# Kernel tuning notes

Hardware: AMD Instinct MI355X
Metric: run time of the kernel (lower is better)

Reference implementation:

```python
import jax, jax.numpy as jnp
import numpy as np

NUM = 512
SIGMA = 0.2

def approx_heaviside(x):
    # ApproxHeaviside forward: hard step (0/1); sigma only affects the surrogate gradient.
    return (x > 0).astype(x.dtype)

def setup_inputs() -> dict:
    key = jax.random.key(0)
    k1, k2 = jax.random.split(key)
    inputs = jax.random.normal(k1, (8, 4096, NUM), dtype=jnp.float32)
    w = jax.random.normal(k2, (NUM, NUM), dtype=jnp.float32) * 0.02
    b = jnp.zeros((NUM,), dtype=jnp.float32)
    return {"inputs": inputs, "w": w, "b": b}

def reference(inputs, w, b):
    # zero the diagonal of w (fill_diagonal_(0))
    w1 = w * (1.0 - jnp.eye(NUM, dtype=w.dtype))
    # inhib = rinputs @ w1 + b over all tokens, vectorized
    inhib = jnp.einsum('bsn,nm->bsm', inputs, w1) + b
    gate = approx_heaviside(inhib)
    # diag_embed(inhib) then matmul == elementwise multiply by the gate
    return inputs * gate
```

## Files before the change

### kernel.cpp

```cpp
#include <hip/hip_runtime.h>
#include <stdint.h>


#define NUMD 512
#define EPS 1e-3f
#define FIXCAP (1u << 20)
#define LCAP 2048u
#define SA 4096.0f
#define SW 8192.0f
#define INV_S (1.0f / 33554432.0f)
#define TILE_F16 4096
#define SLAB_F16 (16 * TILE_F16)

typedef _Float16 f16;
typedef _Float16 f16x8 __attribute__((ext_vector_type(8)));
typedef float    f32x4 __attribute__((ext_vector_type(4)));

#define GLOAD_LDS16(g, l)                                                      \
  __builtin_amdgcn_global_load_lds(                                            \
      (const __attribute__((address_space(1))) void*)(g),                      \
      (__attribute__((address_space(3))) void*)(l), 16, 0, 0)

__global__ __launch_bounds__(256) void prep(
    const float* __restrict__ W, float* __restrict__ Wt,
    f16* __restrict__ WtH, f16* __restrict__ WtL, unsigned* __restrict__ cnt,
    const float* __restrict__ A, f16* __restrict__ AH, f16* __restrict__ AL,
    int M, int nAblocks)
{
    const int b = blockIdx.x;
    if (b < NUMD) {
        const int n = b;
        if (n == 0 && threadIdx.x == 0) *cnt = 0;
        const int slab = n >> 7, rn = n & 127;
        const int srow = (rn >> 1) & 3;
        for (int k = threadIdx.x; k < NUMD; k += 256) {
            float v = W[(size_t)k * NUMD + n];
            if (k == n) v = 0.0f;
            Wt[(size_t)n * NUMD + k] = v;
            const float vs = v * SW;
            f16 h  = (f16)vs;
            f16 lo = (f16)(vs - (float)h);
            const int kt = k >> 5, kk = k & 31, c = kk >> 3, e = kk & 7;
            const int p = c ^ srow;
            const size_t off = (size_t)slab * SLAB_F16 + (size_t)kt * TILE_F16
                             + rn * 32 + p * 8 + e;
            WtH[off] = h; WtL[off] = lo;
        }
    } else {
        const long total = (long)M * 64;
        for (long i = (long)(b - NUMD) * 256 + threadIdx.x; i < total;
             i += (long)nAblocks * 256) {
            const int m = (int)(i >> 6), ch = (int)(i & 63);
            const int kt = ch >> 2, c = ch & 3;
            const int slab = m >> 7, rm = m & 127;
            const int p = c ^ ((rm >> 1) & 3);
            const float* src = A + (size_t)m * NUMD + (ch << 3);
            float4 a0 = *(const float4*)src;
            float4 a1 = *(const float4*)(src + 4);
            const float av[8] = {a0.x, a0.y, a0.z, a0.w, a1.x, a1.y, a1.z, a1.w};
            f16x8 h, lo;
#pragma unroll
            for (int e = 0; e < 8; ++e) {
                const float as = av[e] * SA;
                f16 hv = (f16)as;
                h[e]  = hv;
                lo[e] = (f16)(as - (float)hv);
            }
            const size_t off = (size_t)slab * SLAB_F16 + (size_t)kt * TILE_F16
                             + rm * 32 + p * 8;
            *(f16x8*)(AH + off) = h;
            *(f16x8*)(AL + off) = lo;
        }
    }
}

__global__ __launch_bounds__(256, 2) void li_mfma(
    const float* __restrict__ A,
    const f16* __restrict__ AH, const f16* __restrict__ AL,
    const f16* __restrict__ WtH, const f16* __restrict__ WtL,
    const float* __restrict__ bias,
    float* __restrict__ out,
    unsigned* __restrict__ cnt, unsigned* __restrict__ list,
    int M, int cpx)
{
    __shared__ __align__(16) f16 lds[2][4][128][32];
    __shared__ unsigned lcnt, lbase;

    const int tid = threadIdx.x;
    const int l   = tid & 63;
    const int wv  = tid >> 6;
    const int wr  = wv >> 1;
    const int wc  = wv & 1;
    const int lG  = l >> 4;
    const int lM  = l & 15;

    int w = blockIdx.x;
    if (cpx) { const int xcd = w & 7, c = w >> 3; w = xcd * cpx + c; }
    const int m0  = (w >> 2) * 128;
    const int n0b = (w & 3) * 128;

    const size_t aOff = ((size_t)(m0 >> 7) * SLAB_F16) * 2 + wv * 2048 + l * 16;
    const size_t bOff = ((size_t)(n0b >> 7) * SLAB_F16) * 2 + wv * 2048 + l * 16;
    const char* pAH = (const char*)AH;
    const char* pAL = (const char*)AL;
    const char* pBH = (const char*)WtH;
    const char* pBL = (const char*)WtL;

#define STAGE(nb, ktb) do {                                                    \
    GLOAD_LDS16(pAH + aOff + (ktb),        &lds[nb][0][wv * 32][0]);           \
    GLOAD_LDS16(pAH + aOff + (ktb) + 1024, &lds[nb][0][wv * 32 + 16][0]);      \
    GLOAD_LDS16(pAL + aOff + (ktb),        &lds[nb][1][wv * 32][0]);           \
    GLOAD_LDS16(pAL + aOff + (ktb) + 1024, &lds[nb][1][wv * 32 + 16][0]);      \
    GLOAD_LDS16(pBH + bOff + (ktb),        &lds[nb][2][wv * 32][0]);           \
    GLOAD_LDS16(pBH + bOff + (ktb) + 1024, &lds[nb][2][wv * 32 + 16][0]);      \
    GLOAD_LDS16(pBL + bOff + (ktb),        &lds[nb][3][wv * 32][0]);           \
    GLOAD_LDS16(pBL + bOff + (ktb) + 1024, &lds[nb][3][wv * 32 + 16][0]);      \
  } while (0)

    int aRd[4], bRd[4];
#pragma unroll
    for (int f = 0; f < 4; ++f) {
        const int mr = wr * 64 + f * 16 + lM;
        aRd[f] = mr * 64 + ((lG ^ ((mr >> 1) & 3)) << 4);
        const int nr = wc * 64 + f * 16 + lM;
        bRd[f] = nr * 64 + ((lG ^ ((nr >> 1) & 3)) << 4);
    }

    f32x4 acc[4][4];
#pragma unroll
    for (int i = 0; i < 4; ++i)
#pragma unroll
        for (int j = 0; j < 4; ++j) acc[i][j] = f32x4{0.f, 0.f, 0.f, 0.f};

    STAGE(0, 0);

    const int NT = NUMD / 32;
    for (int kt = 0; kt < NT; ++kt) {
        const int cur = kt & 1;
        __syncthreads();
        if (kt + 1 < NT) STAGE(cur ^ 1, (size_t)(kt + 1) * 8192);

        const char* PAH = (const char*)&lds[cur][0][0][0];
        const char* PAL = (const char*)&lds[cur][1][0][0];
        const char* PBH = (const char*)&lds[cur][2][0][0];
        const char* PBL = (const char*)&lds[cur][3][0][0];

        f16x8 bh[4], bl[4];
#pragma unroll
        for (int fj = 0; fj < 4; ++fj) {
            bh[fj] = *(const f16x8*)(PBH + bRd[fj]);
            bl[fj] = *(const f16x8*)(PBL + bRd[fj]);
        }
        __builtin_amdgcn_s_setprio(1);
#pragma unroll
        for (int fi = 0; fi < 4; ++fi) {
            const f16x8 ah = *(const f16x8*)(PAH + aRd[fi]);
            const f16x8 al = *(const f16x8*)(PAL + aRd[fi]);
#pragma unroll
            for (int fj = 0; fj < 4; ++fj) {
                acc[fi][fj] = __builtin_amdgcn_mfma_f32_16x16x32_f16(ah, bh[fj], acc[fi][fj], 0, 0, 0);
                acc[fi][fj] = __builtin_amdgcn_mfma_f32_16x16x32_f16(ah, bl[fj], acc[fi][fj], 0, 0, 0);
                acc[fi][fj] = __builtin_amdgcn_mfma_f32_16x16x32_f16(al, bh[fj], acc[fi][fj], 0, 0, 0);
            }
        }
        __builtin_amdgcn_s_setprio(0);
    }

    __syncthreads();
    unsigned* lbuf = (unsigned*)&lds[0][0][0][0];
    if (tid == 0) lcnt = 0;
    __syncthreads();

#pragma unroll
    for (int fj = 0; fj < 4; ++fj) {
        const int n = n0b + wc * 64 + fj * 16 + lM;
        const float bvj = bias[n];
#pragma unroll
        for (int fi = 0; fi < 4; ++fi) {
            const int mb = m0 + wr * 64 + fi * 16 + lG * 4;
#pragma unroll
            for (int r = 0; r < 4; ++r) {
                const size_t idx = (size_t)(mb + r) * NUMD + n;
                const float inh = acc[fi][fj][r] * INV_S + bvj;
                const float x = A[idx];
                out[idx] = (inh > 0.0f) ? x : 0.0f;
                if (__builtin_fabsf(inh) <= EPS) {
                    unsigned p = atomicAdd(&lcnt, 1u);
                    if (p < LCAP) lbuf[p] = (unsigned)idx;
                }
            }
        }
    }

    __syncthreads();
    if (tid == 0) {
        unsigned nf = lcnt; if (nf > LCAP) nf = LCAP;
        lbase = atomicAdd(cnt, nf);
    }
    __syncthreads();
    {
        unsigned nf = lcnt; if (nf > LCAP) nf = LCAP;
        for (unsigned i = tid; i < nf; i += 256) {
            const unsigned p = lbase + i;
            if (p < FIXCAP) list[p] = lbuf[i];
        }
    }
#undef STAGE
}

__global__ __launch_bounds__(256) void fixup(
    const float* __restrict__ A, const float* __restrict__ Wt,
    const float* __restrict__ bias, float* __restrict__ out,
    const unsigned* __restrict__ cnt, const unsigned* __restrict__ list,
    unsigned total)
{
    unsigned nfix = *cnt;
    if (nfix > FIXCAP) nfix = FIXCAP;
    for (unsigned e = blockIdx.x * blockDim.x + threadIdx.x; e < nfix;
         e += gridDim.x * blockDim.x) {
        const unsigned code = list[e];
        if (code >= total) continue;
        const int n = (int)(code & 511);
        const float* ar = A  + (size_t)(code >> 9) * NUMD;
        const float* wr = Wt + (size_t)n * NUMD;
        float s = 0.0f;
#pragma unroll 8
        for (int k = 0; k < NUMD; ++k)
            s = fmaf(ar[k], wr[k], s);
        const float inh = s + bias[n];
        out[code] = (inh > 0.0f) ? A[code] : 0.0f;
    }
}

#define BM 128
#define BN 256
#define BK 16
#define TM 8
#define TN 16
#define NTF (NUMD / BK)

__global__ __launch_bounds__(256) void zero_diag_kernel(
    const float* __restrict__ W, float* __restrict__ Wz)
{
    const int f = (int)(blockIdx.x * blockDim.x + threadIdx.x) * 4;
    const int row = f >> 9, col0 = f & 511;
    float4 v = *(const float4*)(W + f);
    if (row == col0 + 0) v.x = 0.0f;
    if (row == col0 + 1) v.y = 0.0f;
    if (row == col0 + 2) v.z = 0.0f;
    if (row == col0 + 3) v.w = 0.0f;
    *(float4*)(Wz + f) = v;
}

template<bool ZDIAG>
__global__ __launch_bounds__(256, 1) void li_gemm_fp32(
    const float* __restrict__ A, const float* __restrict__ Wm,
    const float* __restrict__ bias, float* __restrict__ out, int M)
{
    __shared__ __align__(16) float As[2][BM][BK];
    __shared__ __align__(16) float Bs[2][BK][BN];
    const int tid = threadIdx.x, lane = tid & 63, wv = tid >> 6;
    const int tc = tid & 15, tr = tid >> 4;
    const int m0 = blockIdx.x * BM, n0 = blockIdx.y * BN;
    const int am0 = wv * 32 + (lane >> 2), am1 = am0 + 16;
    const int q0 = ((lane & 3) ^ ((am0 >> 3) & 3)) << 2;
    const int q1 = ((lane & 3) ^ ((am1 >> 3) & 3)) << 2;
    const float* aSrc0 = A + (size_t)(m0 + am0) * NUMD + q0;
    const float* aSrc1 = A + (size_t)(m0 + am1) * NUMD + q1;
    const float* wSrc = Wm + (size_t)(wv * 4) * NUMD + n0 + lane * 4;
    float acc[TM][TN];
#pragma unroll
    for (int i = 0; i < TM; ++i)
#pragma unroll
        for (int j = 0; j < TN; ++j) acc[i][j] = 0.0f;
    GLOAD_LDS16(aSrc0, &As[0][wv * 32][0]);
    GLOAD_LDS16(aSrc1, &As[0][wv * 32 + 16][0]);
#pragma unroll
    for (int r = 0; r < 4; ++r)
        GLOAD_LDS16(wSrc + (size_t)r * NUMD, &Bs[0][wv * 4 + r][0]);
    aSrc0 += BK; aSrc1 += BK; wSrc += (size_t)BK * NUMD;
    for (int kt = 0; kt < NTF; ++kt) {
        const int cur = kt & 1;
        __syncthreads();
        if (kt + 1 < NTF) {
            const int nb = cur ^ 1;
            GLOAD_LDS16(aSrc0, &As[nb][wv * 32][0]);
            GLOAD_LDS16(aSrc1, &As[nb][wv * 32 + 16][0]);
#pragma unroll
            for (int r = 0; r < 4; ++r)
                GLOAD_LDS16(wSrc + (size_t)r * NUMD, &Bs[nb][wv * 4 + r][0]);
            aSrc0 += BK; aSrc1 += BK; wSrc += (size_t)BK * NUMD;
        }
        if (ZDIAG) {
            const int kk = kt * BK;
            if (tid < BK) {
                const int col = kk + tid - n0;
                if (col >= 0 && col < BN) Bs[cur][tid][col] = 0.0f;
            }
            __syncthreads();
        }
#pragma unroll
        for (int g = 0; g < 4; ++g) {
            float4 af[TM];
#pragma unroll
            for (int i = 0; i < TM; ++i) {
                const int m = tr * TM + i;
                af[i] = *(const float4*)&As[cur][m][(g ^ ((m >> 3) & 3)) << 2];
            }
#pragma unroll
            for (int dk = 0; dk < 4; ++dk) {
                float b[TN];
#pragma unroll
                for (int c = 0; c < 4; ++c) {
                    float4 b4 = *(const float4*)&Bs[cur][g * 4 + dk][tc * 4 + 64 * c];
                    b[4*c+0] = b4.x; b[4*c+1] = b4.y; b[4*c+2] = b4.z; b[4*c+3] = b4.w;
                }
#pragma unroll
                for (int i = 0; i < TM; ++i) {
                    const float a = ((const float*)&af[i])[dk];
#pragma unroll
                    for (int j = 0; j < TN; ++j) acc[i][j] = fmaf(a, b[j], acc[i][j]);
                }
            }
        }
    }
    float bv[TN];
#pragma unroll
    for (int c = 0; c < 4; ++c) {
        float4 b4 = *(const float4*)(bias + n0 + tc * 4 + 64 * c);
        bv[4*c+0] = b4.x; bv[4*c+1] = b4.y; bv[4*c+2] = b4.z; bv[4*c+3] = b4.w;
    }
#pragma unroll
    for (int i = 0; i < TM; ++i) {
        const int gm = m0 + tr * TM + i;
        const float* inrow = A + (size_t)gm * NUMD + n0 + tc * 4;
        float* orow = out + (size_t)gm * NUMD + n0 + tc * 4;
#pragma unroll
        for (int c = 0; c < 4; ++c) {
            float4 x = *(const float4*)(inrow + 64 * c);
            float4 o;
            o.x = (acc[i][4*c+0] + bv[4*c+0] > 0.0f) ? x.x : 0.0f;
            o.y = (acc[i][4*c+1] + bv[4*c+1] > 0.0f) ? x.y : 0.0f;
            o.z = (acc[i][4*c+2] + bv[4*c+2] > 0.0f) ? x.z : 0.0f;
            o.w = (acc[i][4*c+3] + bv[4*c+3] > 0.0f) ? x.w : 0.0f;
            *(float4*)(orow + 64 * c) = o;
        }
    }
}

extern "C" void kernel_launch(void* const* d_in, const int* in_sizes, int n_in,
                              void* d_out, int out_size, void* d_ws, size_t ws_size,
                              hipStream_t stream) {
    const float* A    = (const float*)d_in[0];
    const float* W    = (const float*)d_in[1];
    const float* bias = (const float*)d_in[2];
    float* out        = (float*)d_out;
    const int M = in_sizes[0] / NUMD;

    const size_t szA  = (size_t)M * NUMD * 2;
    const size_t need = (2u << 20) + 2 * szA + 1024 + 4 * (size_t)FIXCAP;

    if (ws_size >= need) {
        char* wsb = (char*)d_ws;
        float*    Wt   = (float*)wsb;
        f16*      WtH  = (f16*)(wsb + (1u << 20));
        f16*      WtL  = (f16*)(wsb + (1u << 20) + (512u << 10));
        f16*      AH   = (f16*)(wsb + (2u << 20));
        f16*      AL   = (f16*)(wsb + (2u << 20) + szA);
        unsigned* cnt  = (unsigned*)(wsb + (2u << 20) + 2 * szA);
        unsigned* list = cnt + 256;

        const int nAblocks = 4096;
        prep<<<dim3(NUMD + nAblocks), 256, 0, stream>>>(
            W, Wt, WtH, WtL, cnt, A, AH, AL, M, nAblocks);
        const int nwg = (M / 128) * (NUMD / 128);
        const int cpx = (nwg % 8 == 0) ? (nwg / 8) : 0;
        li_mfma<<<dim3(nwg), 256, 0, stream>>>(A, AH, AL, WtH, WtL, bias, out,
                                               cnt, list, M, cpx);
        fixup<<<dim3(256), 256, 0, stream>>>(A, Wt, bias, out, cnt, list,
                                             (unsigned)((size_t)M * NUMD));
    } else {
        dim3 grid(M / BM, NUMD / BN);
        const size_t wbytes = (size_t)NUMD * NUMD * sizeof(float);
        if (ws_size >= wbytes) {
            float* Wz = (float*)d_ws;
            zero_diag_kernel<<<dim3(NUMD * NUMD / (4 * 256)), 256, 0, stream>>>(W, Wz);
            li_gemm_fp32<false><<<grid, 256, 0, stream>>>(A, Wz, bias, out, M);
        } else {
            li_gemm_fp32<true><<<grid, 256, 0, stream>>>(A, W, bias, out, M);
        }
    }
}
```

Baseline: 241.7 us.

## Fuse A fp32-to-split-f16 conversion into GEMM mainloop, drop prep pass over A

Result: faster. 230.8 us (-4.5%).

```diff
diff --git a/kernel.cpp b/kernel.cpp
--- a/kernel.cpp
+++ b/kernel.cpp
@@ -23,60 +23,29 @@
 
 __global__ __launch_bounds__(256) void prep(
     const float* __restrict__ W, float* __restrict__ Wt,
-    f16* __restrict__ WtH, f16* __restrict__ WtL, unsigned* __restrict__ cnt,
-    const float* __restrict__ A, f16* __restrict__ AH, f16* __restrict__ AL,
-    int M, int nAblocks)
-{
-    const int b = blockIdx.x;
-    if (b < NUMD) {
-        const int n = b;
-        if (n == 0 && threadIdx.x == 0) *cnt = 0;
-        const int slab = n >> 7, rn = n & 127;
-        const int srow = (rn >> 1) & 3;
-        for (int k = threadIdx.x; k < NUMD; k += 256) {
-            float v = W[(size_t)k * NUMD + n];
-            if (k == n) v = 0.0f;
-            Wt[(size_t)n * NUMD + k] = v;
-            const float vs = v * SW;
-            f16 h  = (f16)vs;
-            f16 lo = (f16)(vs - (float)h);
-            const int kt = k >> 5, kk = k & 31, c = kk >> 3, e = kk & 7;
-            const int p = c ^ srow;
-            const size_t off = (size_t)slab * SLAB_F16 + (size_t)kt * TILE_F16
-                             + rn * 32 + p * 8 + e;
-            WtH[off] = h; WtL[off] = lo;
-        }
-    } else {
-        const long total = (long)M * 64;
-        for (long i = (long)(b - NUMD) * 256 + threadIdx.x; i < total;
-             i += (long)nAblocks * 256) {
-            const int m = (int)(i >> 6), ch = (int)(i & 63);
-            const int kt = ch >> 2, c = ch & 3;
-            const int slab = m >> 7, rm = m & 127;
-            const int p = c ^ ((rm >> 1) & 3);
-            const float* src = A + (size_t)m * NUMD + (ch << 3);
-            float4 a0 = *(const float4*)src;
-            float4 a1 = *(const float4*)(src + 4);
-            const float av[8] = {a0.x, a0.y, a0.z, a0.w, a1.x, a1.y, a1.z, a1.w};
-            f16x8 h, lo;
-#pragma unroll
-            for (int e = 0; e < 8; ++e) {
-                const float as = av[e] * SA;
-                f16 hv = (f16)as;
-                h[e]  = hv;
-                lo[e] = (f16)(as - (float)hv);
-            }
-            const size_t off = (size_t)slab * SLAB_F16 + (size_t)kt * TILE_F16
-                             + rm * 32 + p * 8;
-            *(f16x8*)(AH + off) = h;
-            *(f16x8*)(AL + off) = lo;
-        }
+    f16* __restrict__ WtH, f16* __restrict__ WtL, unsigned* __restrict__ cnt)
+{
+    const int n = blockIdx.x;
+    if (n == 0 && threadIdx.x == 0) *cnt = 0;
+    const int slab = n >> 7, rn = n & 127;
+    const int srow = (rn >> 1) & 3;
+    for (int k = threadIdx.x; k < NUMD; k += 256) {
+        float v = W[(size_t)k * NUMD + n];
+        if (k == n) v = 0.0f;
+        Wt[(size_t)n * NUMD + k] = v;
+        const float vs = v * SW;
+        f16 h  = (f16)vs;
+        f16 lo = (f16)(vs - (float)h);
+        const int kt = k >> 5, kk = k & 31, c = kk >> 3, e = kk & 7;
+        const int p = c ^ srow;
+        const size_t off = (size_t)slab * SLAB_F16 + (size_t)kt * TILE_F16
+                         + rn * 32 + p * 8 + e;
+        WtH[off] = h; WtL[off] = lo;
     }
 }
 
 __global__ __launch_bounds__(256, 2) void li_mfma(
     const float* __restrict__ A,
-    const f16* __restrict__ AH, const f16* __restrict__ AL,
     const f16* __restrict__ WtH, const f16* __restrict__ WtL,
     const float* __restrict__ bias,
     float* __restrict__ out,
@@ -99,24 +68,52 @@
     const int m0  = (w >> 2) * 128;
     const int n0b = (w & 3) * 128;
 
-    const size_t aOff = ((size_t)(m0 >> 7) * SLAB_F16) * 2 + wv * 2048 + l * 16;
     const size_t bOff = ((size_t)(n0b >> 7) * SLAB_F16) * 2 + wv * 2048 + l * 16;
-    const char* pAH = (const char*)AH;
-    const char* pAL = (const char*)AL;
     const char* pBH = (const char*)WtH;
     const char* pBL = (const char*)WtL;
 
-#define STAGE(nb, ktb) do {                                                    \
-    GLOAD_LDS16(pAH + aOff + (ktb),        &lds[nb][0][wv * 32][0]);           \
-    GLOAD_LDS16(pAH + aOff + (ktb) + 1024, &lds[nb][0][wv * 32 + 16][0]);      \
-    GLOAD_LDS16(pAL + aOff + (ktb),        &lds[nb][1][wv * 32][0]);           \
-    GLOAD_LDS16(pAL + aOff + (ktb) + 1024, &lds[nb][1][wv * 32 + 16][0]);      \
+#define STAGE_B(nb, ktb) do {                                                  \
     GLOAD_LDS16(pBH + bOff + (ktb),        &lds[nb][2][wv * 32][0]);           \
     GLOAD_LDS16(pBH + bOff + (ktb) + 1024, &lds[nb][2][wv * 32 + 16][0]);      \
     GLOAD_LDS16(pBL + bOff + (ktb),        &lds[nb][3][wv * 32][0]);           \
     GLOAD_LDS16(pBL + bOff + (ktb) + 1024, &lds[nb][3][wv * 32 + 16][0]);      \
   } while (0)
 
+    const int r0 = tid >> 2, ca = tid & 3;
+    const int r1 = r0 + 64;
+    const float* aBase0 = A + (size_t)(m0 + r0) * NUMD + ca * 8;
+    const float* aBase1 = A + (size_t)(m0 + r1) * NUMD + ca * 8;
+    const int wo0 = r0 * 64 + ((ca ^ ((r0 >> 1) & 3)) << 4);
+    const int wo1 = r1 * 64 + ((ca ^ ((r1 >> 1) & 3)) << 4);
+
+    float4 av00, av01, av10, av11;
+
+#define ALOAD(kt) do {                                                         \
+    const float* s0 = aBase0 + (size_t)(kt) * 32;                              \
+    const float* s1 = aBase1 + (size_t)(kt) * 32;                              \
+    av00 = *(const float4*)s0; av01 = *(const float4*)(s0 + 4);                \
+    av10 = *(const float4*)s1; av11 = *(const float4*)(s1 + 4);                \
+  } while (0)
+
+#define ACONV(nb) do {                                                         \
+    const float a0[8] = {av00.x, av00.y, av00.z, av00.w,                       \
+                         av01.x, av01.y, av01.z, av01.w};                      \
+    const float a1[8] = {av10.x, av10.y, av10.z, av10.w,                       \
+                         av11.x, av11.y, av11.z, av11.w};                      \
+    f16x8 h0, lo0, h1, lo1;                                                    \
+    _Pragma("unroll")                                                          \
+    for (int e = 0; e < 8; ++e) {                                              \
+        float as0 = a0[e] * SA; f16 hv0 = (f16)as0;                            \
+        h0[e] = hv0; lo0[e] = (f16)(as0 - (float)hv0);                         \
+        float as1 = a1[e] * SA; f16 hv1 = (f16)as1;                            \
+        h1[e] = hv1; lo1[e] = (f16)(as1 - (float)hv1);                         \
+    }                                                                          \
+    *(f16x8*)((char*)&lds[nb][0][0][0] + wo0) = h0;                            \
+    *(f16x8*)((char*)&lds[nb][1][0][0] + wo0) = lo0;                           \
+    *(f16x8*)((char*)&lds[nb][0][0][0] + wo1) = h1;                            \
+    *(f16x8*)((char*)&lds[nb][1][0][0] + wo1) = lo1;                           \
+  } while (0)
+
     int aRd[4], bRd[4];
 #pragma unroll
     for (int f = 0; f < 4; ++f) {
@@ -132,13 +129,19 @@
 #pragma unroll
         for (int j = 0; j < 4; ++j) acc[i][j] = f32x4{0.f, 0.f, 0.f, 0.f};
 
-    STAGE(0, 0);
+    ALOAD(0);
+    STAGE_B(0, 0);
+    ACONV(0);
 
     const int NT = NUMD / 32;
     for (int kt = 0; kt < NT; ++kt) {
         const int cur = kt & 1;
         __syncthreads();
-        if (kt + 1 < NT) STAGE(cur ^ 1, (size_t)(kt + 1) * 8192);
+
+        if (kt + 1 < NT) {
+            STAGE_B(cur ^ 1, (size_t)(kt + 1) * 8192);
+            ALOAD(kt + 1);
+        }
 
         const char* PAH = (const char*)&lds[cur][0][0][0];
         const char* PAL = (const char*)&lds[cur][1][0][0];
@@ -164,6 +167,8 @@
             }
         }
         __builtin_amdgcn_s_setprio(0);
+
+        if (kt + 1 < NT) ACONV(cur ^ 1);
     }
 
     __syncthreads();
@@ -205,7 +210,9 @@
             if (p < FIXCAP) list[p] = lbuf[i];
         }
     }
-#undef STAGE
+#undef STAGE_B
+#undef ALOAD
+#undef ACONV
 }
 
 __global__ __launch_bounds__(256) void fixup(
@@ -357,25 +364,20 @@
     float* out        = (float*)d_out;
     const int M = in_sizes[0] / NUMD;
 
-    const size_t szA  = (size_t)M * NUMD * 2;
-    const size_t need = (2u << 20) + 2 * szA + 1024 + 4 * (size_t)FIXCAP;
+    const size_t need = (2u << 20) + 1024 + 4 * (size_t)FIXCAP + 4096;
 
     if (ws_size >= need) {
         char* wsb = (char*)d_ws;
         float*    Wt   = (float*)wsb;
         f16*      WtH  = (f16*)(wsb + (1u << 20));
         f16*      WtL  = (f16*)(wsb + (1u << 20) + (512u << 10));
-        f16*      AH   = (f16*)(wsb + (2u << 20));
-        f16*      AL   = (f16*)(wsb + (2u << 20) + szA);
-        unsigned* cnt  = (unsigned*)(wsb + (2u << 20) + 2 * szA);
+        unsigned* cnt  = (unsigned*)(wsb + (2u << 20));
         unsigned* list = cnt + 256;
 
-        const int nAblocks = 4096;
-        prep<<<dim3(NUMD + nAblocks), 256, 0, stream>>>(
-            W, Wt, WtH, WtL, cnt, A, AH, AL, M, nAblocks);
+        prep<<<dim3(NUMD), 256, 0, stream>>>(W, Wt, WtH, WtL, cnt);
         const int nwg = (M / 128) * (NUMD / 128);
         const int cpx = (nwg % 8 == 0) ? (nwg / 8) : 0;
-        li_mfma<<<dim3(nwg), 256, 0, stream>>>(A, AH, AL, WtH, WtL, bias, out,
+        li_mfma<<<dim3(nwg), 256, 0, stream>>>(A, WtH, WtL, bias, out,
                                                cnt, list, M, cpx);
         fixup<<<dim3(256), 256, 0, stream>>>(A, Wt, bias, out, cnt, list,
                                              (unsigned)((size_t)M * NUMD));
```
